# Optimization experiments

Measured on AMD Instinct MI355X. Metric: run time of the kernel, lower is better.

The kernel has to match this reference:

```python
import jax, jax.numpy as jnp
import numpy as np

B, T, S, D, H = 4, 1024, 1024, 1024, 16
DH = D // H  # head dim = 64
EPS = 1e-5
NEG = -1e9  # finite stand-in for -inf (grad-safe)


def setup_inputs() -> dict:
    key = jax.random.key(0)
    ks = jax.random.split(key, 9)
    std = D ** -0.5
    return {
        "q": jax.random.normal(ks[0], (B, T, D), jnp.float32),
        "k": jax.random.normal(ks[1], (B, S, D), jnp.float32),
        "v": jax.random.normal(ks[2], (B, S, D), jnp.float32),
        "attn_mask": jax.random.randint(ks[3], (T, S), 0, 2) == 1,
        "attn_bias": jax.random.normal(ks[4], (H, T, S), jnp.float32) * 0.1,
        "Wq": jax.random.normal(ks[5], (D, D), jnp.float32) * std,
        "Wk": jax.random.normal(ks[6], (D, D), jnp.float32) * std,
        "Wv": jax.random.normal(ks[7], (D, D), jnp.float32) * std,
        "Wo": jax.random.normal(ks[8], (D, D), jnp.float32) * std,
    }


def reference(q, k, v, attn_mask, attn_bias, Wq, Wk, Wv, Wo):
    # project and split heads: [B,T,D] -> [B,H,T,DH]
    qh = (q @ Wq.T).reshape(B, T, H, DH).transpose(0, 2, 1, 3) * (DH ** -0.5)
    kh = (k @ Wk.T).reshape(B, S, H, DH).transpose(0, 2, 1, 3)
    vh = (v @ Wv.T).reshape(B, S, H, DH).transpose(0, 2, 1, 3)
    # scores [B,H,T,S] with bias broadcast over batch, mask over (B,H)
    attn = jnp.einsum('bhtd,bhsd->bhts', qh, kh) + attn_bias
    attn = jnp.where(attn_mask, NEG, attn)
    # inverted softmax: normalize jointly over (heads, target) for each source pos
    a = jax.nn.softmax(attn.reshape(B, H * T, S), axis=1).reshape(B, H, T, S)
    a = jnp.where(attn_mask, 0.0, a)
    a = a / (a.sum(axis=-1, keepdims=True) + EPS)
    out = jnp.einsum('bhts,bhsd->bhtd', a, vh).transpose(0, 2, 1, 3).reshape(B, T, D)
    return out @ Wo.T
```

## Files before the change

kernel.cpp:

```cpp
#include <hip/hip_runtime.h>
#include <hip/hip_bf16.h>
#include <math.h>
#include <stdint.h>

#define B_ 4
#define T_ 1024
#define S_ 1024
#define D_ 1024
#define H_ 16
#define DH_ 64

static constexpr float EPSV = 1e-5f;
static constexpr float LOG2E = 1.4426950408889634f;
static constexpr float NEG2 = -1.4426950e9f;
static constexpr float SCALE_Q = 0.125f * LOG2E;

typedef __attribute__((ext_vector_type(8))) short short8;
typedef __attribute__((ext_vector_type(4))) float f32x4;

#define MFMA_BF16 __builtin_amdgcn_mfma_f32_16x16x32_bf16

__device__ __forceinline__ ushort f2bf(float f) {
  union { float f; unsigned u; } v; v.f = f;
  unsigned r = (v.u + 0x7FFFu + ((v.u >> 16) & 1u)) >> 16;
  return (ushort)r;
}
__device__ __forceinline__ float bf2f(ushort u) {
  union { unsigned u; float f; } v; v.u = (unsigned)u << 16;
  return v.f;
}
__device__ __forceinline__ float exp2_fast(float x) {
  float r;
  asm("v_exp_f32 %0, %1" : "=v"(r) : "v"(x));
  return r;
}
__device__ __forceinline__ unsigned cvt_pk_bf16(float lo, float hi) {
  unsigned r;
  asm("v_cvt_pk_bf16_f32 %0, %1, %2" : "=v"(r) : "v"(lo), "v"(hi));
  return r;
}

__device__ __forceinline__ void gl_lds16(const ushort* g, ushort* l) {
  __builtin_amdgcn_global_load_lds(
      (const __attribute__((address_space(1))) unsigned int*)g,
      (__attribute__((address_space(3))) unsigned int*)l, 16, 0, 0);
}

__global__ __launch_bounds__(256) void k_prep(
    const float* __restrict__ q, const float* __restrict__ k,
    const float* __restrict__ v, const float* __restrict__ Wq,
    const float* __restrict__ Wk, const float* __restrict__ Wv,
    const float* __restrict__ Wo, const float* __restrict__ bias,
    const int* __restrict__ mask, ushort* __restrict__ qb,
    ushort* __restrict__ kb, ushort* __restrict__ vb,
    ushort* __restrict__ Wqb, ushort* __restrict__ Wkb,
    ushort* __restrict__ Wvb, ushort* __restrict__ Wob,
    ushort* __restrict__ bm) {
  const int bid = blockIdx.x;
  if (bid < 12288) {
    const int which = bid >> 12, local = bid & 4095;
    const float* src = (which == 0) ? q : (which == 1) ? k : v;
    ushort* dst = (which == 0) ? qb : (which == 1) ? kb : vb;
    const int i = (local * 256 + threadIdx.x) * 4;
    float4 t = *(const float4*)(src + i);
    *(ushort4*)(dst + i) = make_ushort4(f2bf(t.x), f2bf(t.y), f2bf(t.z), f2bf(t.w));
  } else if (bid < 16384) {
    const int wv_ = bid - 12288;
    const int which = wv_ >> 10, local = wv_ & 1023;
    const float* src = (which == 0) ? Wq : (which == 1) ? Wk : (which == 2) ? Wv : Wo;
    ushort* dst = (which == 0) ? Wqb : (which == 1) ? Wkb : (which == 2) ? Wvb : Wob;
    const int i = (local * 256 + threadIdx.x) * 4;
    float4 t = *(const float4*)(src + i);
    *(ushort4*)(dst + i) = make_ushort4(f2bf(t.x), f2bf(t.y), f2bf(t.z), f2bf(t.w));
  } else {
    const size_t i = ((size_t)(bid - 16384) * 256 + threadIdx.x) * 8;
    const size_t mi = i & (size_t)(T_ * S_ - 1);
    float4 b0 = *(const float4*)(bias + i);
    float4 b1 = *(const float4*)(bias + i + 4);
    int4 m0 = *(const int4*)(mask + mi);
    int4 m1 = *(const int4*)(mask + mi + 4);
    ushort o[8];
    o[0] = f2bf(m0.x ? NEG2 : b0.x * LOG2E); o[1] = f2bf(m0.y ? NEG2 : b0.y * LOG2E);
    o[2] = f2bf(m0.z ? NEG2 : b0.z * LOG2E); o[3] = f2bf(m0.w ? NEG2 : b0.w * LOG2E);
    o[4] = f2bf(m1.x ? NEG2 : b1.x * LOG2E); o[5] = f2bf(m1.y ? NEG2 : b1.y * LOG2E);
    o[6] = f2bf(m1.z ? NEG2 : b1.z * LOG2E); o[7] = f2bf(m1.w ? NEG2 : b1.w * LOG2E);
    *(uint4*)(bm + i) = *(uint4*)o;
  }
}

template <int MODE>
__global__ __launch_bounds__(256) void k_gemm(const ushort* __restrict__ A,
                                              const ushort* __restrict__ W,
                                              void* __restrict__ Yv,
                                              float scale) {
  __shared__ ushort At[128][32];
  __shared__ ushort Wt[128][32];
  const int tid = threadIdx.x;
  const int l = tid & 63, w = tid >> 6;
  const int wm = (w >> 1) * 64, wn = (w & 1) * 64;
  const int r16 = l & 15, g = l >> 4;
  const int i0 = blockIdx.x * 128, j0 = blockIdx.y * 128;
  const int srow = (l >> 2), scol = (l & 3) << 3;
  f32x4 acc[4][4] = {};

  for (int k0 = 0; k0 < D_; k0 += 32) {
    __syncthreads();
#pragma unroll
    for (int u = 0; u < 2; ++u) {
      const int row = w * 32 + u * 16 + srow;
      gl_lds16(&A[(size_t)(i0 + row) * D_ + k0 + scol], &At[w * 32 + u * 16][0]);
      gl_lds16(&W[(size_t)(j0 + row) * D_ + k0 + scol], &Wt[w * 32 + u * 16][0]);
    }
    __syncthreads();
    short8 a0[4], b0[4];
#pragma unroll
    for (int i = 0; i < 4; ++i) a0[i] = *(const short8*)&At[wm + 16 * i + r16][g * 8];
#pragma unroll
    for (int j = 0; j < 4; ++j) b0[j] = *(const short8*)&Wt[wn + 16 * j + r16][g * 8];
#pragma unroll
    for (int i = 0; i < 4; ++i)
#pragma unroll
      for (int j = 0; j < 4; ++j)
        acc[i][j] = MFMA_BF16(a0[i], b0[j], acc[i][j], 0, 0, 0);
  }

#pragma unroll
  for (int i = 0; i < 4; ++i)
#pragma unroll
    for (int j = 0; j < 4; ++j) {
      if (MODE == 2) {
        const int row0 = i0 + wm + 16 * i + 4 * g;
        const int col = j0 + wn + 16 * j + r16;
        const int bb = row0 >> 10, s = row0 & 1023;
        const int hh = col >> 6, dh = col & 63;
        ushort4 pw;
        pw.x = f2bf(acc[i][j][0] * scale); pw.y = f2bf(acc[i][j][1] * scale);
        pw.z = f2bf(acc[i][j][2] * scale); pw.w = f2bf(acc[i][j][3] * scale);
        *(ushort4*)&((ushort*)Yv)[((size_t)(bb * H_ + hh) * DH_ + dh) * 1024 + s] = pw;
      } else {
#pragma unroll
        for (int r = 0; r < 4; ++r) {
          const int row = i0 + wm + 16 * i + 4 * g + r;
          const int col = j0 + wn + 16 * j + r16;
          const float vv = acc[i][j][r] * scale;
          if (MODE == 0) {
            ((float*)Yv)[(size_t)row * D_ + col] = vv;
          } else {
            const int b = row >> 10, t = row & 1023;
            const int h = col >> 6, dh = col & 63;
            ((ushort*)Yv)[(((size_t)(b * H_ + h) * 1024) + t) * DH_ + dh] = f2bf(vv);
          }
        }
      }
    }
}

__global__ __launch_bounds__(256, 4) void k_colstats(const ushort* __restrict__ Qh,
                                                     const ushort* __restrict__ Kh,
                                                     const ushort* __restrict__ biasm,
                                                     float* __restrict__ pc) {
  __shared__ ushort Qt[128][72];
  __shared__ ushort U[9216];
  ushort (*Kt)[72] = (ushort(*)[72])U;
  typedef ushort Row144[144];
  Row144* Bm0 = (Row144*)U;
  Row144* Bm1 = (Row144*)(U + 4608);

  const int bid = blockIdx.x;
  const int x8 = bid & 7;
  const int b = (bid >> 3) & 3;
  const int v = (bid >> 5) * 8 + x8;
  const int h = v >> 6, st = (v >> 3) & 7, tt = v & 7;
  const int s0 = st * 128, t0 = tt * 128;
  const int tid = threadIdx.x, l = tid & 63, w = tid >> 6;
  const int r16 = l & 15, g = l >> 4;

  const ushort* qsrc = Qh + ((size_t)((b * H_ + h) * 1024) + t0) * DH_;
  const ushort* ksrc = Kh + ((size_t)((b * H_ + h) * 1024) + s0) * DH_;
#pragma unroll
  for (int u = 0; u < 4; ++u) {
    const int lin = u * 256 + tid;
    const int row = lin >> 3, c8 = (lin & 7) << 3;
    *(uint4*)&Qt[row][c8] = *(const uint4*)&qsrc[(size_t)row * DH_ + c8];
    *(uint4*)&Kt[row][c8] = *(const uint4*)&ksrc[(size_t)row * DH_ + c8];
  }
  __syncthreads();

  f32x4 acc[8][2] = {};
  __builtin_amdgcn_s_setprio(1);
#pragma unroll
  for (int kc = 0; kc < 2; ++kc) {
    short8 bk0 = *(const short8*)&Kt[w * 32 + r16][kc * 32 + g * 8];
    short8 bk1 = *(const short8*)&Kt[w * 32 + 16 + r16][kc * 32 + g * 8];
#pragma unroll
    for (int i = 0; i < 8; ++i) {
      short8 a = *(const short8*)&Qt[16 * i + r16][kc * 32 + g * 8];
      acc[i][0] = MFMA_BF16(a, bk0, acc[i][0], 0, 0, 0);
      acc[i][1] = MFMA_BF16(a, bk1, acc[i][1], 0, 0, 0);
    }
  }
  __builtin_amdgcn_s_setprio(0);
  __syncthreads();

  const ushort* bsrc = biasm + ((size_t)h * 1024 + t0) * 1024 + s0;
#pragma unroll
  for (int u = 0; u < 2; ++u) {
    const int lin = u * 256 + tid;
    const int row = lin >> 4, c8 = (lin & 15) << 3;
    *(uint4*)&Bm0[row][c8] = *(const uint4*)&bsrc[(size_t)row * 1024 + c8];
  }
  __syncthreads();

  float cs0 = 0.f, cs1 = 0.f;
  const int col0 = w * 32 + r16;
#pragma unroll
  for (int c = 0; c < 4; ++c) {
    Row144* cur = (c & 1) ? Bm1 : Bm0;
    if (c < 3) {
      Row144* nxt = (c & 1) ? Bm0 : Bm1;
#pragma unroll
      for (int u = 0; u < 2; ++u) {
        const int lin = u * 256 + tid;
        const int row = lin >> 4, c8 = (lin & 15) << 3;
        *(uint4*)&nxt[row][c8] =
            *(const uint4*)&bsrc[(size_t)((c + 1) * 32 + row) * 1024 + c8];
      }
    }
#pragma unroll
    for (int ii = 0; ii < 2; ++ii) {
      const int i = 2 * c + ii;
      const int lrow = 16 * ii + 4 * g;
#pragma unroll
      for (int r = 0; r < 4; ++r) {
        cs0 += exp2_fast(acc[i][0][r] + bf2f(cur[lrow + r][col0]));
        cs1 += exp2_fast(acc[i][1][r] + bf2f(cur[lrow + r][col0 + 16]));
      }
    }
    __syncthreads();
  }

  cs0 += __shfl_xor(cs0, 16); cs0 += __shfl_xor(cs0, 32);
  cs1 += __shfl_xor(cs1, 16); cs1 += __shfl_xor(cs1, 32);
  if (g == 0) {
    const size_t base = ((size_t)b * 1024 + s0 + col0) * 128 + h * 8 + tt;
    pc[base] = cs0;
    pc[base + 16 * 128] = cs1;
  }
}

__global__ __launch_bounds__(128) void k_combine(const float* __restrict__ pc,
                                                 float* __restrict__ Civ) {
  const int bs = blockIdx.x, tid = threadIdx.x;
  float c = pc[(size_t)bs * 128 + tid];
  __shared__ float sc[128];
  sc[tid] = c;
  __syncthreads();
  for (int off = 64; off > 0; off >>= 1) {
    if (tid < off) sc[tid] += sc[tid + off];
    __syncthreads();
  }
  if (tid == 0) {
    const float C = sc[0];
    Civ[bs] = (C > 0.f) ? 1.f / C : 0.f;
  }
}

__global__ __launch_bounds__(256, 2) void k_attn(const ushort* __restrict__ Qh,
                                                 const ushort* __restrict__ Kh,
                                                 const ushort* __restrict__ VhT,
                                                 const ushort* __restrict__ biasm,
                                                 const float* __restrict__ Civ,
                                                 ushort* __restrict__ O) {
  __shared__ ushort Kt[128][68];
  __shared__ ushort VtT[64][132];
  __shared__ ushort BmPt[128][132];
  __shared__ float Cih[128];
  __shared__ float Rp[4][128];

  const int bid = blockIdx.x;
  const int tt = bid >> 6;
  const int bh = bid & 63;
  const int b = bh >> 4, h = bh & 15;
  const int t0 = tt * 128;

  const int tid = threadIdx.x, l = tid & 63, w = tid >> 6;
  const int r16 = l & 15, g = l >> 4;
  const size_t kvbase = (size_t)bh * 1024 * DH_;
  const size_t vbase  = (size_t)bh * DH_ * 1024;

  short8 aq[8][2];
#pragma unroll
  for (int i = 0; i < 8; ++i) {
    const ushort* qr = Qh + ((size_t)bh * 1024 + t0 + 16 * i + r16) * DH_;
    aq[i][0] = *(const short8*)(qr + g * 8);
    aq[i][1] = *(const short8*)(qr + 32 + g * 8);
  }

  f32x4 aco[2][4] = {};
  float rloc[8] = {};

#pragma unroll 1
  for (int sc = 0; sc < 8; ++sc) {
    const int s0c = sc * 128;
    __syncthreads();

    {
      const ushort* ksrc = Kh + kvbase + (size_t)s0c * DH_;
#pragma unroll
      for (int u = 0; u < 4; ++u) {
        const int lin = u * 256 + tid;
        const int row = lin >> 3, c8 = (lin & 7) << 3;
        *(uint4*)&Kt[row][c8] = *(const uint4*)&ksrc[(size_t)row * DH_ + c8];
      }
      const ushort* vsrc = VhT + vbase + s0c;
#pragma unroll
      for (int u = 0; u < 4; ++u) {
        const int lin = u * 256 + tid;
        const int row = lin >> 4, c8 = (lin & 15) << 3;
        *(uint4*)&VtT[row][c8] = *(const uint4*)&vsrc[(size_t)row * 1024 + c8];
      }
      const ushort* bsrc = biasm + ((size_t)h * 1024 + t0) * 1024 + s0c;
#pragma unroll
      for (int u = 0; u < 8; ++u) {
        const int lin = u * 256 + tid;
        const int row = lin >> 4, c8 = (lin & 15) << 3;
        *(uint4*)&BmPt[row][c8] = *(const uint4*)&bsrc[(size_t)row * 1024 + c8];
      }
      if (tid < 128) Cih[tid] = Civ[(size_t)b * 1024 + s0c + tid];
    }
    __syncthreads();

#pragma unroll
    for (int j2 = 0; j2 < 2; ++j2) {
      const int jf = 2 * w + j2;
      f32x4 as[8] = {};
      short8 kf0 = *(const short8*)&Kt[16 * jf + r16][g * 8];
      short8 kf1 = *(const short8*)&Kt[16 * jf + r16][32 + g * 8];
      __builtin_amdgcn_s_setprio(1);
#pragma unroll
      for (int i = 0; i < 8; ++i) {
        as[i] = MFMA_BF16(kf0, aq[i][0], as[i], 0, 0, 0);
        as[i] = MFMA_BF16(kf1, aq[i][1], as[i], 0, 0, 0);
      }
      __builtin_amdgcn_s_setprio(0);
      const int scol = 16 * jf + 4 * g;
      const float4 cv = *(const float4*)&Cih[scol];
#pragma unroll
      for (int i = 0; i < 8; ++i) {
        const int srow = 16 * i + r16;
        ushort4 bv4 = *(const ushort4*)&BmPt[srow][scol];
        const float p0 = exp2_fast(as[i][0] + bf2f(bv4.x)) * cv.x;
        const float p1 = exp2_fast(as[i][1] + bf2f(bv4.y)) * cv.y;
        const float p2 = exp2_fast(as[i][2] + bf2f(bv4.z)) * cv.z;
        const float p3 = exp2_fast(as[i][3] + bf2f(bv4.w)) * cv.w;
        rloc[i] += (p0 + p1) + (p2 + p3);
        uint2 pw;
        pw.x = cvt_pk_bf16(p0, p1);
        pw.y = cvt_pk_bf16(p2, p3);
        *(uint2*)&BmPt[srow][scol] = pw;
      }
    }
    __syncthreads();

    __builtin_amdgcn_s_setprio(1);
#pragma unroll
    for (int rg = 0; rg < 2; ++rg) {
#pragma unroll
      for (int kc = 0; kc < 4; ++kc) {
        short8 ap = *(const short8*)&BmPt[32 * w + 16 * rg + r16][kc * 32 + g * 8];
#pragma unroll
        for (int j = 0; j < 4; ++j) {
          short8 bv = *(const short8*)&VtT[16 * j + r16][kc * 32 + g * 8];
          aco[rg][j] = MFMA_BF16(ap, bv, aco[rg][j], 0, 0, 0);
        }
      }
    }
    __builtin_amdgcn_s_setprio(0);
  }

#pragma unroll
  for (int i = 0; i < 8; ++i) {
    float vsum = rloc[i];
    vsum += __shfl_xor(vsum, 16);
    vsum += __shfl_xor(vsum, 32);
    if (l < 16) Rp[w][16 * i + r16] = vsum;
  }
  __syncthreads();

#pragma unroll
  for (int rg = 0; rg < 2; ++rg)
#pragma unroll
    for (int j = 0; j < 4; ++j)
#pragma unroll
      for (int r = 0; r < 4; ++r) {
        const int tl = 32 * w + 16 * rg + 4 * g + r;
        const float R = Rp[0][tl] + Rp[1][tl] + Rp[2][tl] + Rp[3][tl];
        const float o = aco[rg][j][r] / (R + EPSV);
        const int d = 16 * j + r16;
        O[((size_t)(b * 1024) + t0 + tl) * D_ + h * DH_ + d] = f2bf(o);
      }
}

extern "C" void kernel_launch(void* const* d_in, const int* in_sizes, int n_in,
                              void* d_out, int out_size, void* d_ws, size_t ws_size,
                              hipStream_t stream) {
  (void)in_sizes; (void)n_in; (void)out_size; (void)ws_size;
  const float* q    = (const float*)d_in[0];
  const float* k    = (const float*)d_in[1];
  const float* v    = (const float*)d_in[2];
  const int*   mask = (const int*)d_in[3];
  const float* bias = (const float*)d_in[4];
  const float* Wq   = (const float*)d_in[5];
  const float* Wk   = (const float*)d_in[6];
  const float* Wv   = (const float*)d_in[7];
  const float* Wo   = (const float*)d_in[8];
  float* out = (float*)d_out;

  ushort* qb   = (ushort*)d_ws;
  ushort* kb   = qb + 4194304;
  ushort* vb   = kb + 4194304;
  ushort* Wqb  = vb + 4194304;
  ushort* Wkb  = Wqb + 1048576;
  ushort* Wvb  = Wkb + 1048576;
  ushort* Wob  = Wvb + 1048576;
  ushort* Qh   = Wob + 1048576;
  ushort* Kh   = Qh + 4194304;
  ushort* VhT  = Kh + 4194304;
  ushort* Ob   = VhT + 4194304;
  ushort* bm   = Ob + 4194304;
  float*  pc   = (float*)(bm + 16777216);
  float*  Civ  = pc + 524288;

  k_prep<<<24576, 256, 0, stream>>>(q, k, v, Wq, Wk, Wv, Wo, bias, mask,
                                    qb, kb, vb, Wqb, Wkb, Wvb, Wob, bm);

  k_gemm<1><<<dim3(32, 8), 256, 0, stream>>>(qb, Wqb, Qh, SCALE_Q);
  k_gemm<1><<<dim3(32, 8), 256, 0, stream>>>(kb, Wkb, Kh, 1.0f);
  k_gemm<2><<<dim3(32, 8), 256, 0, stream>>>(vb, Wvb, VhT, 1.0f);

  k_colstats<<<4096, 256, 0, stream>>>(Qh, Kh, bm, pc);
  k_combine<<<4096, 128, 0, stream>>>(pc, Civ);
  k_attn<<<512, 256, 0, stream>>>(Qh, Kh, VhT, bm, Civ, Ob);

  k_gemm<0><<<dim3(32, 8), 256, 0, stream>>>(Ob, Wob, out, 1.0f);
}
```

Before: 191.2 us.

## Fuse input bf16 conversion into projection GEMMs and bias/mask prep into colstats

Removes the big prep kernel. The q/k/v fp32 inputs are now converted to bf16 inside the projection GEMM's LDS staging, with a padded LDS stride. The bias+mask to bf16 log2-scaled conversion moves into k_colstats, where blocks with b==0 also write the bm buffer that k_attn uses later. This drops the bf16 copies of q/k/v and one full pass over bias. In exchange the GEMM A-loads become register-staged instead of direct-to-LDS, and colstats now reads fp32 bias plus the int mask for every batch, roughly four times the bias bytes it read before.

Result: slower. 216.0 us (+13.0%).

```diff
diff --git a/kernel.cpp b/kernel.cpp
--- a/kernel.cpp
+++ b/kernel.cpp
@@ -46,54 +46,29 @@
       (__attribute__((address_space(3))) unsigned int*)l, 16, 0, 0);
 }
 
-__global__ __launch_bounds__(256) void k_prep(
-    const float* __restrict__ q, const float* __restrict__ k,
-    const float* __restrict__ v, const float* __restrict__ Wq,
-    const float* __restrict__ Wk, const float* __restrict__ Wv,
-    const float* __restrict__ Wo, const float* __restrict__ bias,
-    const int* __restrict__ mask, ushort* __restrict__ qb,
-    ushort* __restrict__ kb, ushort* __restrict__ vb,
-    ushort* __restrict__ Wqb, ushort* __restrict__ Wkb,
-    ushort* __restrict__ Wvb, ushort* __restrict__ Wob,
-    ushort* __restrict__ bm) {
-  const int bid = blockIdx.x;
-  if (bid < 12288) {
-    const int which = bid >> 12, local = bid & 4095;
-    const float* src = (which == 0) ? q : (which == 1) ? k : v;
-    ushort* dst = (which == 0) ? qb : (which == 1) ? kb : vb;
-    const int i = (local * 256 + threadIdx.x) * 4;
-    float4 t = *(const float4*)(src + i);
-    *(ushort4*)(dst + i) = make_ushort4(f2bf(t.x), f2bf(t.y), f2bf(t.z), f2bf(t.w));
-  } else if (bid < 16384) {
-    const int wv_ = bid - 12288;
-    const int which = wv_ >> 10, local = wv_ & 1023;
-    const float* src = (which == 0) ? Wq : (which == 1) ? Wk : (which == 2) ? Wv : Wo;
-    ushort* dst = (which == 0) ? Wqb : (which == 1) ? Wkb : (which == 2) ? Wvb : Wob;
-    const int i = (local * 256 + threadIdx.x) * 4;
-    float4 t = *(const float4*)(src + i);
-    *(ushort4*)(dst + i) = make_ushort4(f2bf(t.x), f2bf(t.y), f2bf(t.z), f2bf(t.w));
-  } else {
-    const size_t i = ((size_t)(bid - 16384) * 256 + threadIdx.x) * 8;
-    const size_t mi = i & (size_t)(T_ * S_ - 1);
-    float4 b0 = *(const float4*)(bias + i);
-    float4 b1 = *(const float4*)(bias + i + 4);
-    int4 m0 = *(const int4*)(mask + mi);
-    int4 m1 = *(const int4*)(mask + mi + 4);
-    ushort o[8];
-    o[0] = f2bf(m0.x ? NEG2 : b0.x * LOG2E); o[1] = f2bf(m0.y ? NEG2 : b0.y * LOG2E);
-    o[2] = f2bf(m0.z ? NEG2 : b0.z * LOG2E); o[3] = f2bf(m0.w ? NEG2 : b0.w * LOG2E);
-    o[4] = f2bf(m1.x ? NEG2 : b1.x * LOG2E); o[5] = f2bf(m1.y ? NEG2 : b1.y * LOG2E);
-    o[6] = f2bf(m1.z ? NEG2 : b1.z * LOG2E); o[7] = f2bf(m1.w ? NEG2 : b1.w * LOG2E);
-    *(uint4*)(bm + i) = *(uint4*)o;
-  }
-}
-
-template <int MODE>
-__global__ __launch_bounds__(256) void k_gemm(const ushort* __restrict__ A,
+__global__ __launch_bounds__(256) void k_prepW(const float* __restrict__ Wq,
+                                               const float* __restrict__ Wk,
+                                               const float* __restrict__ Wv,
+                                               const float* __restrict__ Wo,
+                                               ushort* __restrict__ Wqb,
+                                               ushort* __restrict__ Wkb,
+                                               ushort* __restrict__ Wvb,
+                                               ushort* __restrict__ Wob) {
+  const int which = blockIdx.x >> 10, local = blockIdx.x & 1023;
+  const float* src = (which == 0) ? Wq : (which == 1) ? Wk : (which == 2) ? Wv : Wo;
+  ushort* dst = (which == 0) ? Wqb : (which == 1) ? Wkb : (which == 2) ? Wvb : Wob;
+  const int i = (local * 256 + threadIdx.x) * 4;
+  float4 t = *(const float4*)(src + i);
+  *(ushort4*)(dst + i) = make_ushort4(f2bf(t.x), f2bf(t.y), f2bf(t.z), f2bf(t.w));
+}
+
+template <int MODE, bool AF32>
+__global__ __launch_bounds__(256) void k_gemm(const void* __restrict__ Av,
                                               const ushort* __restrict__ W,
                                               void* __restrict__ Yv,
                                               float scale) {
-  __shared__ ushort At[128][32];
+  constexpr int AST = AF32 ? 40 : 32;
+  __shared__ ushort At[128][AST];
   __shared__ ushort Wt[128][32];
   const int tid = threadIdx.x;
   const int l = tid & 63, w = tid >> 6;
@@ -108,8 +83,26 @@
 #pragma unroll
     for (int u = 0; u < 2; ++u) {
       const int row = w * 32 + u * 16 + srow;
-      gl_lds16(&A[(size_t)(i0 + row) * D_ + k0 + scol], &At[w * 32 + u * 16][0]);
       gl_lds16(&W[(size_t)(j0 + row) * D_ + k0 + scol], &Wt[w * 32 + u * 16][0]);
+      if (!AF32) {
+        gl_lds16(&((const ushort*)Av)[(size_t)(i0 + row) * D_ + k0 + scol],
+                 &At[w * 32 + u * 16][0]);
+      }
+    }
+    if (AF32) {
+      const float* A32 = (const float*)Av;
+#pragma unroll
+      for (int u = 0; u < 2; ++u) {
+        const int lin = u * 256 + tid;
+        const int row = lin >> 2, c8 = (lin & 3) << 3;
+        const float* src = &A32[(size_t)(i0 + row) * D_ + k0 + c8];
+        float4 f0 = *(const float4*)src;
+        float4 f1 = *(const float4*)(src + 4);
+        uint4 pk;
+        pk.x = cvt_pk_bf16(f0.x, f0.y); pk.y = cvt_pk_bf16(f0.z, f0.w);
+        pk.z = cvt_pk_bf16(f1.x, f1.y); pk.w = cvt_pk_bf16(f1.z, f1.w);
+        *(uint4*)&At[row][c8] = pk;
+      }
     }
     __syncthreads();
     short8 a0[4], b0[4];
@@ -155,14 +148,43 @@
     }
 }
 
+typedef ushort Row144[144];
+__device__ __forceinline__ void stage_fuse(Row144* dst, const float* bsrc,
+                                           const int* msrc, ushort* bmdst,
+                                           int crow0, int tid, bool wr) {
+#pragma unroll
+  for (int u = 0; u < 2; ++u) {
+    const int lin = u * 256 + tid;
+    const int row = lin >> 4, c8 = (lin & 15) << 3;
+    const size_t go = (size_t)(crow0 + row) * 1024 + c8;
+    float4 f0 = *(const float4*)(bsrc + go);
+    float4 f1 = *(const float4*)(bsrc + go + 4);
+    int4 m0 = *(const int4*)(msrc + go);
+    int4 m1 = *(const int4*)(msrc + go + 4);
+    ushort o[8];
+    o[0] = f2bf(m0.x ? NEG2 : f0.x * LOG2E);
+    o[1] = f2bf(m0.y ? NEG2 : f0.y * LOG2E);
+    o[2] = f2bf(m0.z ? NEG2 : f0.z * LOG2E);
+    o[3] = f2bf(m0.w ? NEG2 : f0.w * LOG2E);
+    o[4] = f2bf(m1.x ? NEG2 : f1.x * LOG2E);
+    o[5] = f2bf(m1.y ? NEG2 : f1.y * LOG2E);
+    o[6] = f2bf(m1.z ? NEG2 : f1.z * LOG2E);
+    o[7] = f2bf(m1.w ? NEG2 : f1.w * LOG2E);
+    const uint4 pk = *(uint4*)o;
+    *(uint4*)&dst[row][c8] = pk;
+    if (wr) *(uint4*)(bmdst + go) = pk;
+  }
+}
+
 __global__ __launch_bounds__(256, 4) void k_colstats(const ushort* __restrict__ Qh,
                                                      const ushort* __restrict__ Kh,
-                                                     const ushort* __restrict__ biasm,
-                                                     float* __restrict__ pc) {
+                                                     const float* __restrict__ bias,
+                                                     const int* __restrict__ mask,
+                                                     float* __restrict__ pc,
+                                                     ushort* __restrict__ bm) {
   __shared__ ushort Qt[128][72];
   __shared__ ushort U[9216];
   ushort (*Kt)[72] = (ushort(*)[72])U;
-  typedef ushort Row144[144];
   Row144* Bm0 = (Row144*)U;
   Row144* Bm1 = (Row144*)(U + 4608);
 
@@ -202,13 +224,12 @@
   __builtin_amdgcn_s_setprio(0);
   __syncthreads();
 
-  const ushort* bsrc = biasm + ((size_t)h * 1024 + t0) * 1024 + s0;
-#pragma unroll
-  for (int u = 0; u < 2; ++u) {
-    const int lin = u * 256 + tid;
-    const int row = lin >> 4, c8 = (lin & 15) << 3;
-    *(uint4*)&Bm0[row][c8] = *(const uint4*)&bsrc[(size_t)row * 1024 + c8];
-  }
+  const float* bsrc = bias + ((size_t)h * 1024 + t0) * 1024 + s0;
+  const int* msrc = mask + (size_t)t0 * 1024 + s0;
+  ushort* bmdst = bm + ((size_t)h * 1024 + t0) * 1024 + s0;
+  const bool wr = (b == 0);
+
+  stage_fuse(Bm0, bsrc, msrc, bmdst, 0, tid, wr);
   __syncthreads();
 
   float cs0 = 0.f, cs1 = 0.f;
@@ -218,13 +239,7 @@
     Row144* cur = (c & 1) ? Bm1 : Bm0;
     if (c < 3) {
       Row144* nxt = (c & 1) ? Bm0 : Bm1;
-#pragma unroll
-      for (int u = 0; u < 2; ++u) {
-        const int lin = u * 256 + tid;
-        const int row = lin >> 4, c8 = (lin & 15) << 3;
-        *(uint4*)&nxt[row][c8] =
-            *(const uint4*)&bsrc[(size_t)((c + 1) * 32 + row) * 1024 + c8];
-      }
+      stage_fuse(nxt, bsrc, msrc, bmdst, (c + 1) * 32, tid, wr);
     }
 #pragma unroll
     for (int ii = 0; ii < 2; ++ii) {
@@ -416,10 +431,7 @@
   const float* Wo   = (const float*)d_in[8];
   float* out = (float*)d_out;
 
-  ushort* qb   = (ushort*)d_ws;
-  ushort* kb   = qb + 4194304;
-  ushort* vb   = kb + 4194304;
-  ushort* Wqb  = vb + 4194304;
+  ushort* Wqb  = (ushort*)d_ws;
   ushort* Wkb  = Wqb + 1048576;
   ushort* Wvb  = Wkb + 1048576;
   ushort* Wob  = Wvb + 1048576;
@@ -431,16 +443,15 @@
   float*  pc   = (float*)(bm + 16777216);
   float*  Civ  = pc + 524288;
 
-  k_prep<<<24576, 256, 0, stream>>>(q, k, v, Wq, Wk, Wv, Wo, bias, mask,
-                                    qb, kb, vb, Wqb, Wkb, Wvb, Wob, bm);
-
-  k_gemm<1><<<dim3(32, 8), 256, 0, stream>>>(qb, Wqb, Qh, SCALE_Q);
-  k_gemm<1><<<dim3(32, 8), 256, 0, stream>>>(kb, Wkb, Kh, 1.0f);
-  k_gemm<2><<<dim3(32, 8), 256, 0, stream>>>(vb, Wvb, VhT, 1.0f);
-
-  k_colstats<<<4096, 256, 0, stream>>>(Qh, Kh, bm, pc);
+  k_prepW<<<4096, 256, 0, stream>>>(Wq, Wk, Wv, Wo, Wqb, Wkb, Wvb, Wob);
+
+  k_gemm<1, true><<<dim3(32, 8), 256, 0, stream>>>(q, Wqb, Qh, SCALE_Q);
+  k_gemm<1, true><<<dim3(32, 8), 256, 0, stream>>>(k, Wkb, Kh, 1.0f);
+  k_gemm<2, true><<<dim3(32, 8), 256, 0, stream>>>(v, Wvb, VhT, 1.0f);
+
+  k_colstats<<<4096, 256, 0, stream>>>(Qh, Kh, bias, mask, pc, bm);
   k_combine<<<4096, 128, 0, stream>>>(pc, Civ);
   k_attn<<<512, 256, 0, stream>>>(Qh, Kh, VhT, bm, Civ, Ob);
 
-  k_gemm<0><<<dim3(32, 8), 256, 0, stream>>>(Ob, Wob, out, 1.0f);
-}
+  k_gemm<0, false><<<dim3(32, 8), 256, 0, stream>>>(Ob, Wob, out, 1.0f);
+}
```
